# Kernel optimization log

Measured on AMD Instinct MI355X. Metric: run time of the kernel, lower is better.

## Reference

```python
import jax, jax.numpy as jnp
import numpy as np

N_NODES = 50000
N_EDGES = 800000
D_IN, D_HID, D_OUT = 64, 128, 64


def _glorot(key, fan_in, fan_out):
    lim = (6.0 / (fan_in + fan_out)) ** 0.5
    return jax.random.uniform(key, (fan_in, fan_out), jnp.float32, -lim, lim)


def setup_inputs() -> dict:
    key = jax.random.key(0)
    ks = jax.random.split(key, 10)
    x = jax.random.normal(ks[0], (N_NODES, D_IN), jnp.float32)
    edge_index = jax.random.randint(ks[1], (2, N_EDGES), 0, N_NODES, jnp.int64)
    # GINConv1 MLP: Linear(D_IN->D_HID), ReLU, Linear(D_HID->D_HID)
    W1a = _glorot(ks[2], D_IN, D_HID); b1a = jnp.zeros((D_HID,), jnp.float32)
    W1b = _glorot(ks[3], D_HID, D_HID); b1b = jnp.zeros((D_HID,), jnp.float32)
    # GINConv2 MLP: Linear(D_HID->D_HID), ReLU, Linear(D_HID->D_OUT)
    W2a = _glorot(ks[4], D_HID, D_HID); b2a = jnp.zeros((D_HID,), jnp.float32)
    W2b = _glorot(ks[5], D_HID, D_OUT); b2b = jnp.zeros((D_OUT,), jnp.float32)
    return {"x": x, "edge_index": edge_index,
            "W1a": W1a, "b1a": b1a, "W1b": W1b, "b1b": b1b,
            "W2a": W2a, "b2a": b2a, "W2b": W2b, "b2b": b2b}


def _gin_conv(x, src, dst, Wa, ba, Wb, bb):
    # GIN aggregation (eps = 0): h_i = x_i + sum_{j in N(i)} x_j
    msgs = x[src]                                   # [E, d] gather
    agg = jax.ops.segment_sum(msgs, dst, num_segments=x.shape[0])  # [N, d]
    h = x + agg
    # 2-layer MLP
    h = jax.nn.relu(h @ Wa + ba)
    return h @ Wb + bb


def reference(x, edge_index, W1a, b1a, W1b, b1b, W2a, b2a, W2b, b2b):
    src, dst = edge_index[0], edge_index[1]
    h = jax.nn.relu(_gin_conv(x, src, dst, W1a, b1a, W1b, b1b))
    h = jax.nn.relu(_gin_conv(h, src, dst, W2a, b2a, W2b, b2b))
    return h
```

## Files before the change

### kernel.cpp

```cpp
#include <hip/hip_runtime.h>

#define N_NODES 50000
#define N_EDGES 800000

typedef __attribute__((ext_vector_type(8))) short short8;
typedef __attribute__((ext_vector_type(4))) float floatx4;

static __device__ __forceinline__ unsigned short f2b(float f) {
    unsigned int u = __float_as_uint(f);
    unsigned int r = u + 0x7fffu + ((u >> 16) & 1u);
    return (unsigned short)(r >> 16);
}
static __device__ __forceinline__ unsigned int pk(float a, float b) {
    return (unsigned)f2b(a) | ((unsigned)f2b(b) << 16);
}
static __device__ __forceinline__ float blo(unsigned int u) {
    return __uint_as_float(u << 16);
}
static __device__ __forceinline__ float bhi(unsigned int u) {
    return __uint_as_float(u & 0xffff0000u);
}

static __device__ __forceinline__ void acc4(float* f, uint4 v0, uint4 v1,
                                            uint4 v2, uint4 v3) {
    f[0] += (blo(v0.x) + blo(v1.x)) + (blo(v2.x) + blo(v3.x));
    f[1] += (bhi(v0.x) + bhi(v1.x)) + (bhi(v2.x) + bhi(v3.x));
    f[2] += (blo(v0.y) + blo(v1.y)) + (blo(v2.y) + blo(v3.y));
    f[3] += (bhi(v0.y) + bhi(v1.y)) + (bhi(v2.y) + bhi(v3.y));
    f[4] += (blo(v0.z) + blo(v1.z)) + (blo(v2.z) + blo(v3.z));
    f[5] += (bhi(v0.z) + bhi(v1.z)) + (bhi(v2.z) + bhi(v3.z));
    f[6] += (blo(v0.w) + blo(v1.w)) + (blo(v2.w) + blo(v3.w));
    f[7] += (bhi(v0.w) + bhi(v1.w)) + (bhi(v2.w) + bhi(v3.w));
}

__global__ void hist_rank_kernel(const int* __restrict__ dst,
                                 int* __restrict__ deg, int* __restrict__ rank,
                                 int n) {
    int i = blockIdx.x * blockDim.x + threadIdx.x;
    if (i < n) rank[i] = atomicAdd(&deg[dst[i]], 1);
}

__global__ __launch_bounds__(1024) void offsets_kernel(
    const int* __restrict__ deg, int* __restrict__ offpd,
    int* __restrict__ gcount, unsigned short* __restrict__ nbr, int n) {
    __shared__ int s[1024];
    __shared__ int base;
    const int tid = threadIdx.x;
    const int i = blockIdx.x * 1024 + tid;
    const int d = (i < n) ? deg[i] : 0;
    const int pd = (d + 3) & ~3;
    s[tid] = pd;
    __syncthreads();
    for (int o = 1; o < 1024; o <<= 1) {
        int t = (tid >= o) ? s[tid - o] : 0;
        __syncthreads();
        s[tid] += t;
        __syncthreads();
    }
    if (tid == 1023) base = atomicAdd(gcount, s[1023]);
    __syncthreads();
    const int excl = base + s[tid] - pd;
    if (i < n) {
        offpd[i] = (excl << 10) | pd;
        for (int k = d; k < pd; ++k) nbr[excl + k] = (unsigned short)N_NODES;
    }
}

__global__ void fill_kernel(const int* __restrict__ src,
                            const int* __restrict__ dst,
                            const int* __restrict__ rank,
                            const int* __restrict__ offpd,
                            unsigned short* __restrict__ nbr, int n) {
    int i = blockIdx.x * blockDim.x + threadIdx.x;
    if (i < n) nbr[(offpd[dst[i]] >> 10) + rank[i]] = (unsigned short)src[i];
}

__global__ __launch_bounds__(256) void prep_kernel(
    const float* __restrict__ W1a, const float* __restrict__ W1b,
    const float* __restrict__ W2a, const float* __restrict__ W2b,
    const float* __restrict__ x, unsigned short* __restrict__ W1aT,
    unsigned short* __restrict__ W1bT, unsigned short* __restrict__ W2aT,
    unsigned short* __restrict__ W2bT, unsigned short* __restrict__ xb,
    unsigned short* __restrict__ h, int* __restrict__ deg,
    int* __restrict__ gcount) {
    int i = blockIdx.x * 256 + threadIdx.x;
    if (i < 8192) {
        int n = i >> 6, k = i & 63;
        W1aT[i] = f2b(W1a[k * 128 + n]);
    } else if (i < 24576) {
        int j = i - 8192, n = j >> 7, k = j & 127;
        W1bT[j] = f2b(W1b[k * 128 + n]);
    } else if (i < 40960) {
        int j = i - 24576, n = j >> 7, k = j & 127;
        W2aT[j] = f2b(W2a[k * 128 + n]);
    } else if (i < 49152) {
        int j = i - 40960, n = j >> 7, k = j & 127;
        W2bT[j] = f2b(W2b[k * 64 + n]);
    } else if (i < 49152 + N_NODES * 16) {
        int j = i - 49152;
        float4 v = ((const float4*)x)[j];
        uint2 o;
        o.x = pk(v.x, v.y);
        o.y = pk(v.z, v.w);
        ((uint2*)xb)[j] = o;
    } else if (i < 49152 + N_NODES * 16 + N_NODES) {
        int j = i - (49152 + N_NODES * 16);
        deg[j] = 0;
        if (j == 0) *gcount = 0;
    } else {
        int j = i - (49152 + N_NODES * 16 + N_NODES);
        uint4 z = {0u, 0u, 0u, 0u};
        if (j < 8)
            ((uint4*)(xb + (size_t)N_NODES * 64))[j] = z;
        else if (j < 24)
            ((uint4*)(h + (size_t)N_NODES * 128))[j - 8] = z;
    }
}

template <int DIN, int DH, int DOUT, bool OUT_BF16>
__global__ __launch_bounds__(256) void gin_fused_kernel(
    const unsigned short* __restrict__ xin, const int* __restrict__ offpd,
    const unsigned short* __restrict__ nbr,
    const unsigned short* __restrict__ WaT, const float* __restrict__ ba,
    const unsigned short* __restrict__ WbT, const float* __restrict__ bb,
    void* __restrict__ outp, int n_rows) {
    constexpr int LPR = DIN / 8;
    constexpr int ROWS = 256 / LPR;
    constexpr int SA = DIN + 16;
    constexpr int SH = DH + 16;
    __shared__ __attribute__((aligned(16))) unsigned short tA[ROWS * SA];
    __shared__ __attribute__((aligned(16))) unsigned short hidA[ROWS * SH];

    const int tid = threadIdx.x;
    const int row0 = blockIdx.x * ROWS;
    const int grp = tid / LPR;
    const int c = tid % LPR;
    const int node = row0 + grp;

    float f[8] = {0.f, 0.f, 0.f, 0.f, 0.f, 0.f, 0.f, 0.f};
    const uint4* xr = (const uint4*)xin;
    if (node < n_rows) {
        const uint4 a = xr[(size_t)node * LPR + c];
        f[0] = blo(a.x); f[1] = bhi(a.x);
        f[2] = blo(a.y); f[3] = bhi(a.y);
        f[4] = blo(a.z); f[5] = bhi(a.z);
        f[6] = blo(a.w); f[7] = bhi(a.w);
        const int v = offpd[node];
        const int lo = v >> 10;
        const int hi = lo + (v & 1023);
        int j = lo;
        for (; j + 8 <= hi; j += 8) {
            const uint2 i0 = *(const uint2*)&nbr[j];
            const uint2 i1 = *(const uint2*)&nbr[j + 4];
            const int s0 = i0.x & 0xffff, s1 = i0.x >> 16;
            const int s2 = i0.y & 0xffff, s3 = i0.y >> 16;
            const int s4 = i1.x & 0xffff, s5 = i1.x >> 16;
            const int s6 = i1.y & 0xffff, s7 = i1.y >> 16;
            const uint4 v0 = xr[(size_t)s0 * LPR + c];
            const uint4 v1 = xr[(size_t)s1 * LPR + c];
            const uint4 v2 = xr[(size_t)s2 * LPR + c];
            const uint4 v3 = xr[(size_t)s3 * LPR + c];
            const uint4 v4 = xr[(size_t)s4 * LPR + c];
            const uint4 v5 = xr[(size_t)s5 * LPR + c];
            const uint4 v6 = xr[(size_t)s6 * LPR + c];
            const uint4 v7 = xr[(size_t)s7 * LPR + c];
            acc4(f, v0, v1, v2, v3);
            acc4(f, v4, v5, v6, v7);
        }
        if (j < hi) {
            const uint2 i0 = *(const uint2*)&nbr[j];
            const int s0 = i0.x & 0xffff, s1 = i0.x >> 16;
            const int s2 = i0.y & 0xffff, s3 = i0.y >> 16;
            const uint4 v0 = xr[(size_t)s0 * LPR + c];
            const uint4 v1 = xr[(size_t)s1 * LPR + c];
            const uint4 v2 = xr[(size_t)s2 * LPR + c];
            const uint4 v3 = xr[(size_t)s3 * LPR + c];
            acc4(f, v0, v1, v2, v3);
        }
    }
    uint4 o;
    o.x = pk(f[0], f[1]);
    o.y = pk(f[2], f[3]);
    o.z = pk(f[4], f[5]);
    o.w = pk(f[6], f[7]);
    *(uint4*)&tA[grp * SA + c * 8] = o;
    __syncthreads();

    constexpr int MT = ROWS / 16;
    constexpr int NSPLIT = 4 / MT;
    const int lane = tid & 63;
    const int wv = tid >> 6;
    const int wm = wv % MT;
    const int wn = wv / MT;
    const int quad = lane >> 4;
    const int l16 = lane & 15;
    const int m0 = wm * 16;

    short8 a1[DIN / 32];
#pragma unroll
    for (int kk = 0; kk < DIN / 32; ++kk)
        a1[kk] = *(const short8*)&tA[(m0 + l16) * SA + kk * 32 + quad * 8];
#pragma unroll
    for (int nt = 0; nt < DH / (16 * NSPLIT); ++nt) {
        const int col = wn * (DH / NSPLIT) + nt * 16 + l16;
        floatx4 acc = {0.f, 0.f, 0.f, 0.f};
#pragma unroll
        for (int kk = 0; kk < DIN / 32; ++kk) {
            short8 b = *(const short8*)&WaT[col * DIN + kk * 32 + quad * 8];
            acc = __builtin_amdgcn_mfma_f32_16x16x32_bf16(a1[kk], b, acc, 0, 0, 0);
        }
        const float bias = ba[col];
#pragma unroll
        for (int r = 0; r < 4; ++r) {
            const float v = fmaxf(acc[r] + bias, 0.f);
            hidA[(m0 + quad * 4 + r) * SH + col] = f2b(v);
        }
    }
    __syncthreads();

    short8 a2[DH / 32];
#pragma unroll
    for (int kk = 0; kk < DH / 32; ++kk)
        a2[kk] = *(const short8*)&hidA[(m0 + l16) * SH + kk * 32 + quad * 8];
#pragma unroll
    for (int nt = 0; nt < DOUT / (16 * NSPLIT); ++nt) {
        const int col = wn * (DOUT / NSPLIT) + nt * 16 + l16;
        floatx4 acc = {0.f, 0.f, 0.f, 0.f};
#pragma unroll
        for (int kk = 0; kk < DH / 32; ++kk) {
            short8 b = *(const short8*)&WbT[col * DH + kk * 32 + quad * 8];
            acc = __builtin_amdgcn_mfma_f32_16x16x32_bf16(a2[kk], b, acc, 0, 0, 0);
        }
        const float bias = bb[col];
#pragma unroll
        for (int r = 0; r < 4; ++r) {
            const float v = fmaxf(acc[r] + bias, 0.f);
            const int grow = row0 + m0 + quad * 4 + r;
            if (grow < n_rows) {
                if (OUT_BF16)
                    ((unsigned short*)outp)[(size_t)grow * DOUT + col] = f2b(v);
                else
                    ((float*)outp)[(size_t)grow * DOUT + col] = v;
            }
        }
    }
}

extern "C" void kernel_launch(void* const* d_in, const int* in_sizes, int n_in,
                              void* d_out, int out_size, void* d_ws,
                              size_t ws_size, hipStream_t stream) {
    const float* x   = (const float*)d_in[0];
    const int*   ei  = (const int*)d_in[1];
    const float* W1a = (const float*)d_in[2];
    const float* b1a = (const float*)d_in[3];
    const float* W1b = (const float*)d_in[4];
    const float* b1b = (const float*)d_in[5];
    const float* W2a = (const float*)d_in[6];
    const float* b2a = (const float*)d_in[7];
    const float* W2b = (const float*)d_in[8];
    const float* b2b = (const float*)d_in[9];
    float* out = (float*)d_out;

    const int* src = ei;
    const int* dst = ei + N_EDGES;

    unsigned short* xb = (unsigned short*)d_ws;
    unsigned short* h  = xb + (size_t)(N_NODES + 1) * 64;
    unsigned short* W1aT = h + (size_t)(N_NODES + 1) * 128;
    unsigned short* W1bT = W1aT + 8192;
    unsigned short* W2aT = W1bT + 16384;
    unsigned short* W2bT = W2aT + 16384;
    int* deg    = (int*)(W2bT + 8192);
    int* offpd  = deg + N_NODES;
    int* gcount = offpd + N_NODES;
    int* rank   = gcount + 64;
    unsigned short* nbr = (unsigned short*)(rank + N_EDGES);

    constexpr int NB = (N_NODES + 1023) / 1024;
    constexpr int PREP_THREADS = 49152 + N_NODES * 16 + N_NODES + 24;

    prep_kernel<<<(PREP_THREADS + 255) / 256, 256, 0, stream>>>(
        W1a, W1b, W2a, W2b, x, W1aT, W1bT, W2aT, W2bT, xb, h, deg, gcount);

    hist_rank_kernel<<<(N_EDGES + 255) / 256, 256, 0, stream>>>(dst, deg, rank,
                                                                N_EDGES);
    offsets_kernel<<<NB, 1024, 0, stream>>>(deg, offpd, gcount, nbr, N_NODES);
    fill_kernel<<<(N_EDGES + 255) / 256, 256, 0, stream>>>(src, dst, rank,
                                                           offpd, nbr, N_EDGES);

    gin_fused_kernel<64, 128, 128, true>
        <<<(N_NODES + 31) / 32, 256, 0, stream>>>(xb, offpd, nbr, W1aT, b1a,
                                                  W1bT, b1b, h, N_NODES);

    gin_fused_kernel<128, 128, 64, false>
        <<<(N_NODES + 15) / 16, 256, 0, stream>>>(h, offpd, nbr, W2aT, b2a,
                                                  W2bT, b2b, out, N_NODES);
}
```

Baseline: 217.3 us.

## Use 64-row tiles with 4 lanes per node and multi-pass feature gathering

Each block now handles 64 nodes, with 4 threads per node gathering 32 features per pass and looping over passes for wider inputs. Each wave then owns a 16-row slice across all output columns, so the second barrier between the two MLP layers can be removed. The intent is to amortize the weight loads and block overhead over more rows and to cut synchronization. The cost is fewer threads per node during the gather, so latency per edge is exposed more serially, and the grid is smaller, which lowers occupancy.

Result: slower. 236.9 us (+9.0%).

```diff
diff --git a/kernel.cpp b/kernel.cpp
--- a/kernel.cpp
+++ b/kernel.cpp
@@ -124,8 +124,9 @@
     const unsigned short* __restrict__ WaT, const float* __restrict__ ba,
     const unsigned short* __restrict__ WbT, const float* __restrict__ bb,
     void* __restrict__ outp, int n_rows) {
-    constexpr int LPR = DIN / 8;
-    constexpr int ROWS = 256 / LPR;
+    constexpr int ROWS = 64;
+    constexpr int PASSES = DIN / 32;
+    constexpr int RS = DIN / 8;
     constexpr int SA = DIN + 16;
     constexpr int SH = DH + 16;
     __shared__ __attribute__((aligned(16))) unsigned short tA[ROWS * SA];
@@ -133,76 +134,78 @@
 
     const int tid = threadIdx.x;
     const int row0 = blockIdx.x * ROWS;
-    const int grp = tid / LPR;
-    const int c = tid % LPR;
+    const int grp = tid >> 2;
+    const int c = tid & 3;
     const int node = row0 + grp;
 
-    float f[8] = {0.f, 0.f, 0.f, 0.f, 0.f, 0.f, 0.f, 0.f};
-    const uint4* xr = (const uint4*)xin;
+    int lo = 0, hi = 0;
     if (node < n_rows) {
-        const uint4 a = xr[(size_t)node * LPR + c];
-        f[0] = blo(a.x); f[1] = bhi(a.x);
-        f[2] = blo(a.y); f[3] = bhi(a.y);
-        f[4] = blo(a.z); f[5] = bhi(a.z);
-        f[6] = blo(a.w); f[7] = bhi(a.w);
         const int v = offpd[node];
-        const int lo = v >> 10;
-        const int hi = lo + (v & 1023);
-        int j = lo;
-        for (; j + 8 <= hi; j += 8) {
-            const uint2 i0 = *(const uint2*)&nbr[j];
-            const uint2 i1 = *(const uint2*)&nbr[j + 4];
-            const int s0 = i0.x & 0xffff, s1 = i0.x >> 16;
-            const int s2 = i0.y & 0xffff, s3 = i0.y >> 16;
-            const int s4 = i1.x & 0xffff, s5 = i1.x >> 16;
-            const int s6 = i1.y & 0xffff, s7 = i1.y >> 16;
-            const uint4 v0 = xr[(size_t)s0 * LPR + c];
-            const uint4 v1 = xr[(size_t)s1 * LPR + c];
-            const uint4 v2 = xr[(size_t)s2 * LPR + c];
-            const uint4 v3 = xr[(size_t)s3 * LPR + c];
-            const uint4 v4 = xr[(size_t)s4 * LPR + c];
-            const uint4 v5 = xr[(size_t)s5 * LPR + c];
-            const uint4 v6 = xr[(size_t)s6 * LPR + c];
-            const uint4 v7 = xr[(size_t)s7 * LPR + c];
-            acc4(f, v0, v1, v2, v3);
-            acc4(f, v4, v5, v6, v7);
-        }
-        if (j < hi) {
-            const uint2 i0 = *(const uint2*)&nbr[j];
-            const int s0 = i0.x & 0xffff, s1 = i0.x >> 16;
-            const int s2 = i0.y & 0xffff, s3 = i0.y >> 16;
-            const uint4 v0 = xr[(size_t)s0 * LPR + c];
-            const uint4 v1 = xr[(size_t)s1 * LPR + c];
-            const uint4 v2 = xr[(size_t)s2 * LPR + c];
-            const uint4 v3 = xr[(size_t)s3 * LPR + c];
-            acc4(f, v0, v1, v2, v3);
-        }
-    }
-    uint4 o;
-    o.x = pk(f[0], f[1]);
-    o.y = pk(f[2], f[3]);
-    o.z = pk(f[4], f[5]);
-    o.w = pk(f[6], f[7]);
-    *(uint4*)&tA[grp * SA + c * 8] = o;
+        lo = v >> 10;
+        hi = lo + (v & 1023);
+    }
+
+    for (int q = 0; q < PASSES; ++q) {
+        float f[8] = {0.f, 0.f, 0.f, 0.f, 0.f, 0.f, 0.f, 0.f};
+        const uint4* xr = (const uint4*)xin + q * 4 + c;
+        if (node < n_rows) {
+            const uint4 a = xr[(size_t)node * RS];
+            f[0] = blo(a.x); f[1] = bhi(a.x);
+            f[2] = blo(a.y); f[3] = bhi(a.y);
+            f[4] = blo(a.z); f[5] = bhi(a.z);
+            f[6] = blo(a.w); f[7] = bhi(a.w);
+            int j = lo;
+            for (; j + 8 <= hi; j += 8) {
+                const uint2 i0 = *(const uint2*)&nbr[j];
+                const uint2 i1 = *(const uint2*)&nbr[j + 4];
+                const int s0 = i0.x & 0xffff, s1 = i0.x >> 16;
+                const int s2 = i0.y & 0xffff, s3 = i0.y >> 16;
+                const int s4 = i1.x & 0xffff, s5 = i1.x >> 16;
+                const int s6 = i1.y & 0xffff, s7 = i1.y >> 16;
+                const uint4 v0 = xr[(size_t)s0 * RS];
+                const uint4 v1 = xr[(size_t)s1 * RS];
+                const uint4 v2 = xr[(size_t)s2 * RS];
+                const uint4 v3 = xr[(size_t)s3 * RS];
+                const uint4 v4 = xr[(size_t)s4 * RS];
+                const uint4 v5 = xr[(size_t)s5 * RS];
+                const uint4 v6 = xr[(size_t)s6 * RS];
+                const uint4 v7 = xr[(size_t)s7 * RS];
+                acc4(f, v0, v1, v2, v3);
+                acc4(f, v4, v5, v6, v7);
+            }
+            if (j < hi) {
+                const uint2 i0 = *(const uint2*)&nbr[j];
+                const int s0 = i0.x & 0xffff, s1 = i0.x >> 16;
+                const int s2 = i0.y & 0xffff, s3 = i0.y >> 16;
+                const uint4 v0 = xr[(size_t)s0 * RS];
+                const uint4 v1 = xr[(size_t)s1 * RS];
+                const uint4 v2 = xr[(size_t)s2 * RS];
+                const uint4 v3 = xr[(size_t)s3 * RS];
+                acc4(f, v0, v1, v2, v3);
+            }
+        }
+        uint4 o;
+        o.x = pk(f[0], f[1]);
+        o.y = pk(f[2], f[3]);
+        o.z = pk(f[4], f[5]);
+        o.w = pk(f[6], f[7]);
+        *(uint4*)&tA[grp * SA + q * 32 + c * 8] = o;
+    }
     __syncthreads();
 
-    constexpr int MT = ROWS / 16;
-    constexpr int NSPLIT = 4 / MT;
     const int lane = tid & 63;
     const int wv = tid >> 6;
-    const int wm = wv % MT;
-    const int wn = wv / MT;
     const int quad = lane >> 4;
     const int l16 = lane & 15;
-    const int m0 = wm * 16;
+    const int m0 = wv * 16;
 
     short8 a1[DIN / 32];
 #pragma unroll
     for (int kk = 0; kk < DIN / 32; ++kk)
         a1[kk] = *(const short8*)&tA[(m0 + l16) * SA + kk * 32 + quad * 8];
 #pragma unroll
-    for (int nt = 0; nt < DH / (16 * NSPLIT); ++nt) {
-        const int col = wn * (DH / NSPLIT) + nt * 16 + l16;
+    for (int nt = 0; nt < DH / 16; ++nt) {
+        const int col = nt * 16 + l16;
         floatx4 acc = {0.f, 0.f, 0.f, 0.f};
 #pragma unroll
         for (int kk = 0; kk < DIN / 32; ++kk) {
@@ -216,15 +219,14 @@
             hidA[(m0 + quad * 4 + r) * SH + col] = f2b(v);
         }
     }
-    __syncthreads();
 
     short8 a2[DH / 32];
 #pragma unroll
     for (int kk = 0; kk < DH / 32; ++kk)
         a2[kk] = *(const short8*)&hidA[(m0 + l16) * SH + kk * 32 + quad * 8];
 #pragma unroll
-    for (int nt = 0; nt < DOUT / (16 * NSPLIT); ++nt) {
-        const int col = wn * (DOUT / NSPLIT) + nt * 16 + l16;
+    for (int nt = 0; nt < DOUT / 16; ++nt) {
+        const int col = nt * 16 + l16;
         floatx4 acc = {0.f, 0.f, 0.f, 0.f};
 #pragma unroll
         for (int kk = 0; kk < DH / 32; ++kk) {
@@ -289,10 +291,10 @@
                                                            offpd, nbr, N_EDGES);
 
     gin_fused_kernel<64, 128, 128, true>
-        <<<(N_NODES + 31) / 32, 256, 0, stream>>>(xb, offpd, nbr, W1aT, b1a,
+        <<<(N_NODES + 63) / 64, 256, 0, stream>>>(xb, offpd, nbr, W1aT, b1a,
                                                   W1bT, b1b, h, N_NODES);
 
     gin_fused_kernel<128, 128, 64, false>
-        <<<(N_NODES + 15) / 16, 256, 0, stream>>>(h, offpd, nbr, W2aT, b2a,
+        <<<(N_NODES + 63) / 64, 256, 0, stream>>>(h, offpd, nbr, W2aT, b2a,
                                                   W2bT, b2b, out, N_NODES);
 }
```
